# Kernel optimization log

Measured on AMD Instinct MI355X. Metric: run time of the kernel, lower is better.

Reference implementation:

```python
import jax, jax.numpy as jnp
import numpy as np

MAX_VAL = 10000.0
KS = (1, 5, 10, 20, 50)
B, V, L = 256, 128000, 200


def setup_inputs() -> dict:
    key = jax.random.key(0)
    k1, k2, k3 = jax.random.split(key, 3)
    scores = jax.random.normal(k1, (B, V), dtype=jnp.float32)
    labels = jax.random.randint(k2, (B,), 0, V, dtype=jnp.int64)
    seqs = jax.random.randint(k3, (B, L), 0, V, dtype=jnp.int64)
    return {"scores": scores, "labels": labels, "seqs": seqs}


def reference(scores, labels, seqs):
    b = scores.shape[0]
    rows = jnp.arange(b)
    # gather predicted score for the true label BEFORE masking (torch order)
    predicts = scores[rows, labels]  # [B]
    # scatter -MAX_VAL at history items (masked scatter)
    masked = scores.at[rows[:, None], seqs].set(-MAX_VAL)  # [B, V]
    valid_length = (masked > -MAX_VAL).sum(-1).astype(jnp.float32)  # [B]
    rank = (predicts[:, None] < masked).sum(-1).astype(jnp.float32)  # [B]
    res = []
    for k in KS:
        indicator = (rank < k).astype(jnp.float32)
        res.append((indicator / jnp.log2(rank + 2.0)).mean())  # NDCG@k
        res.append(indicator.mean())  # Recall@k
    res.append((1.0 / (rank + 1.0)).mean())  # MRR
    res.append((1.0 - rank / valid_length).mean())  # AUC-like
    res.append(jnp.float32(0.0))
    return jnp.stack(res)
```

## Files before the change

### kernel.cpp

```cpp
#include <hip/hip_runtime.h>
#include <math.h>

#define B_CONST 256
#define V_CONST 128000
#define L_CONST 200
#define SLICES 4

__global__ void zero_ws_kernel(int* __restrict__ ws) {
    int i = threadIdx.x;
    if (i < 3 * B_CONST) ws[i] = 0;
}

__global__ __launch_bounds__(256) void rank_count_kernel(
    const float* __restrict__ scores,
    const int* __restrict__ labels,
    const int* __restrict__ seqs,
    int* __restrict__ gt,
    int* __restrict__ sub,
    int* __restrict__ distinct)
{
    const int b     = blockIdx.y;
    const int slice = blockIdx.x;
    const int tid   = threadIdx.x;

    const float* row = scores + (size_t)b * V_CONST;
    const int   label   = labels[b];
    const float predict = row[label];

    __shared__ int s_cnt, s_sub, s_dist;
    if (tid == 0) { s_cnt = 0; s_sub = 0; s_dist = 0; }
    __syncthreads();

    const int f4_total = V_CONST / 4;
    const int f4_per   = f4_total / SLICES;
    const float4* row4 = (const float4*)row;
    const int begin = slice * f4_per;
    const int end   = begin + f4_per;
    int local = 0;
    for (int i = begin + tid; i < end; i += 256) {
        float4 v = row4[i];
        local += (v.x > predict) + (v.y > predict) + (v.z > predict) + (v.w > predict);
    }
    #pragma unroll
    for (int off = 32; off > 0; off >>= 1)
        local += __shfl_down(local, off, 64);
    if ((tid & 63) == 0) atomicAdd(&s_cnt, local);

    if (slice == 0 && tid < L_CONST) {
        const int* srow = seqs + b * L_CONST;
        const int s = srow[tid];
        bool first = true;
        for (int j = 0; j < tid; ++j) {
            if (srow[j] == s) { first = false; break; }
        }
        if (first) {
            atomicAdd(&s_dist, 1);
            if (row[s] > predict) atomicAdd(&s_sub, 1);
        }
    }
    __syncthreads();

    if (tid == 0) {
        atomicAdd(&gt[b], s_cnt);
        if (slice == 0) {
            atomicAdd(&sub[b], s_sub);
            atomicAdd(&distinct[b], s_dist);
        }
    }
}

__global__ __launch_bounds__(256) void finalize_kernel(
    const int* __restrict__ gt,
    const int* __restrict__ sub,
    const int* __restrict__ distinct,
    float* __restrict__ out)
{
    const int b = threadIdx.x;
    const float rank  = (float)(gt[b] - sub[b]);
    const float valid = (float)(V_CONST - distinct[b]);

    const float ks[5] = {1.0f, 5.0f, 10.0f, 20.0f, 50.0f};
    float vals[12];
    const float invlog = 1.0f / log2f(rank + 2.0f);
    #pragma unroll
    for (int i = 0; i < 5; ++i) {
        const float ind = (rank < ks[i]) ? 1.0f : 0.0f;
        vals[2 * i]     = ind * invlog;
        vals[2 * i + 1] = ind;
    }
    vals[10] = 1.0f / (rank + 1.0f);
    vals[11] = 1.0f - rank / valid;

    __shared__ float red[4];
    for (int q = 0; q < 12; ++q) {
        float v = vals[q];
        #pragma unroll
        for (int off = 32; off > 0; off >>= 1)
            v += __shfl_down(v, off, 64);
        if ((b & 63) == 0) red[b >> 6] = v;
        __syncthreads();
        if (b == 0) out[q] = (red[0] + red[1] + red[2] + red[3]) * (1.0f / B_CONST);
        __syncthreads();
    }
    if (b == 0) out[12] = 0.0f;
}

extern "C" void kernel_launch(void* const* d_in, const int* in_sizes, int n_in,
                              void* d_out, int out_size, void* d_ws, size_t ws_size,
                              hipStream_t stream) {
    const float* scores = (const float*)d_in[0];
    const int*   labels = (const int*)d_in[1];
    const int*   seqs   = (const int*)d_in[2];
    float* out = (float*)d_out;
    int*   ws  = (int*)d_ws;

    int* gt       = ws;
    int* sub      = ws + B_CONST;
    int* distinct = ws + 2 * B_CONST;

    zero_ws_kernel<<<1, 1024, 0, stream>>>(ws);
    rank_count_kernel<<<dim3(SLICES, B_CONST), 256, 0, stream>>>(
        scores, labels, seqs, gt, sub, distinct);
    finalize_kernel<<<1, 256, 0, stream>>>(gt, sub, distinct, out);
}
```

Measured before the change: 220.5 us.

## Unroll row scan with five loads in flight and drop workspace zeroing kernel

Splits each row into five slices instead of four, and fully unrolls the scan so every thread issues five float4 loads per iteration, giving more memory-level parallelism. Per-slice partial counts are now written to separate workspace slots rather than combined with global atomics, so the zeroing kernel launch is removed and the finalize kernel sums the partials. Launch bounds ask for higher occupancy. The hard-coded constant 6400 ties the indexing to V=128000 and SLICES=5.

Result: faster. 209.5 us (-5.0%).

```diff
diff --git a/kernel.cpp b/kernel.cpp
--- a/kernel.cpp
+++ b/kernel.cpp
@@ -4,47 +4,49 @@
 #define B_CONST 256
 #define V_CONST 128000
 #define L_CONST 200
-#define SLICES 4
+#define SLICES  5
 
-__global__ void zero_ws_kernel(int* __restrict__ ws) {
-    int i = threadIdx.x;
-    if (i < 3 * B_CONST) ws[i] = 0;
-}
 
-__global__ __launch_bounds__(256) void rank_count_kernel(
+__global__ __launch_bounds__(256, 8) void rank_count_kernel(
     const float* __restrict__ scores,
     const int* __restrict__ labels,
     const int* __restrict__ seqs,
-    int* __restrict__ gt,
+    int* __restrict__ partial,
     int* __restrict__ sub,
-    int* __restrict__ distinct)
+    int* __restrict__ dist)
 {
+    const int slice = blockIdx.x;
     const int b     = blockIdx.y;
-    const int slice = blockIdx.x;
     const int tid   = threadIdx.x;
 
     const float* row = scores + (size_t)b * V_CONST;
-    const int   label   = labels[b];
-    const float predict = row[label];
+    const float predict = row[labels[b]];
 
     __shared__ int s_cnt, s_sub, s_dist;
     if (tid == 0) { s_cnt = 0; s_sub = 0; s_dist = 0; }
     __syncthreads();
 
-    const int f4_total = V_CONST / 4;
-    const int f4_per   = f4_total / SLICES;
     const float4* row4 = (const float4*)row;
-    const int begin = slice * f4_per;
-    const int end   = begin + f4_per;
-    int local = 0;
-    for (int i = begin + tid; i < end; i += 256) {
-        float4 v = row4[i];
-        local += (v.x > predict) + (v.y > predict) + (v.z > predict) + (v.w > predict);
+    int idx = slice * 6400 + tid;
+    int cnt = 0;
+    #pragma unroll
+    for (int r = 0; r < 5; ++r) {
+        float4 a0 = row4[idx];
+        float4 a1 = row4[idx + 256];
+        float4 a2 = row4[idx + 512];
+        float4 a3 = row4[idx + 768];
+        float4 a4 = row4[idx + 1024];
+        cnt += (a0.x > predict) + (a0.y > predict) + (a0.z > predict) + (a0.w > predict);
+        cnt += (a1.x > predict) + (a1.y > predict) + (a1.z > predict) + (a1.w > predict);
+        cnt += (a2.x > predict) + (a2.y > predict) + (a2.z > predict) + (a2.w > predict);
+        cnt += (a3.x > predict) + (a3.y > predict) + (a3.z > predict) + (a3.w > predict);
+        cnt += (a4.x > predict) + (a4.y > predict) + (a4.z > predict) + (a4.w > predict);
+        idx += 1280;
     }
     #pragma unroll
     for (int off = 32; off > 0; off >>= 1)
-        local += __shfl_down(local, off, 64);
-    if ((tid & 63) == 0) atomicAdd(&s_cnt, local);
+        cnt += __shfl_down(cnt, off, 64);
+    if ((tid & 63) == 0) atomicAdd(&s_cnt, cnt);
 
     if (slice == 0 && tid < L_CONST) {
         const int* srow = seqs + b * L_CONST;
@@ -61,23 +63,26 @@
     __syncthreads();
 
     if (tid == 0) {
-        atomicAdd(&gt[b], s_cnt);
+        partial[slice * B_CONST + b] = s_cnt;
         if (slice == 0) {
-            atomicAdd(&sub[b], s_sub);
-            atomicAdd(&distinct[b], s_dist);
+            sub[b]  = s_sub;
+            dist[b] = s_dist;
         }
     }
 }
 
 __global__ __launch_bounds__(256) void finalize_kernel(
-    const int* __restrict__ gt,
+    const int* __restrict__ partial,
     const int* __restrict__ sub,
-    const int* __restrict__ distinct,
+    const int* __restrict__ dist,
     float* __restrict__ out)
 {
     const int b = threadIdx.x;
-    const float rank  = (float)(gt[b] - sub[b]);
-    const float valid = (float)(V_CONST - distinct[b]);
+    int gt = 0;
+    #pragma unroll
+    for (int s = 0; s < SLICES; ++s) gt += partial[s * B_CONST + b];
+    const float rank  = (float)(gt - sub[b]);
+    const float valid = (float)(V_CONST - dist[b]);
 
     const float ks[5] = {1.0f, 5.0f, 10.0f, 20.0f, 50.0f};
     float vals[12];
@@ -114,12 +119,11 @@
     float* out = (float*)d_out;
     int*   ws  = (int*)d_ws;
 
-    int* gt       = ws;
-    int* sub      = ws + B_CONST;
-    int* distinct = ws + 2 * B_CONST;
+    int* partial = ws;
+    int* sub     = ws + SLICES * B_CONST;
+    int* dist    = ws + SLICES * B_CONST + B_CONST;
 
-    zero_ws_kernel<<<1, 1024, 0, stream>>>(ws);
     rank_count_kernel<<<dim3(SLICES, B_CONST), 256, 0, stream>>>(
-        scores, labels, seqs, gt, sub, distinct);
-    finalize_kernel<<<1, 256, 0, stream>>>(gt, sub, distinct, out);
+        scores, labels, seqs, partial, sub, dist);
+    finalize_kernel<<<1, 256, 0, stream>>>(partial, sub, dist, out);
 }
```
